# Kernel tuning notes

Measured on AMD Instinct MI355X. Metric: run time of the kernel, lower is better.

The kernel has to match this reference:

```python
import jax, jax.numpy as jnp
import numpy as np

L1, L2, L3, COUNT, B = 3072, 15, 32, 8, 16384

def setup_inputs() -> dict:
    key = jax.random.key(0)
    ks = jax.random.split(key, 10)
    s = 1.0 / np.sqrt(L1)
    inp = {
        'x': jax.random.normal(ks[0], (B, L1), dtype=jnp.float32),
        'ls_indices': jax.random.randint(ks[1], (B,), 0, COUNT, dtype=jnp.int64 if jax.config.jax_enable_x64 else jnp.int32),
        # l1: Linear(L1, (L2+1)*count)
        'l1_w': jax.random.uniform(ks[2], ((L2 + 1) * COUNT, L1), jnp.float32, -s, s),
        'l1_b': jax.random.uniform(ks[3], ((L2 + 1) * COUNT,), jnp.float32, -s, s),
        # l1_fact: Linear(L1, L2+1) -- zero-initialized in the original module
        'l1f_w': jnp.zeros((L2 + 1, L1), jnp.float32),
        'l1f_b': jnp.zeros((L2 + 1,), jnp.float32),
        # l2: Linear(2*L2, L3*count)
        'l2_w': jax.random.uniform(ks[4], (L3 * COUNT, 2 * L2), jnp.float32, -0.18, 0.18),
        'l2_b': jax.random.uniform(ks[5], (L3 * COUNT,), jnp.float32, -0.18, 0.18),
        # output: Linear(L3, count) -- bias zero-initialized
        'out_w': jax.random.uniform(ks[6], (COUNT, L3), jnp.float32, -0.176, 0.176),
        'out_b': jnp.zeros((COUNT,), jnp.float32),
    }
    return inp

def reference(x, ls_indices, l1_w, l1_b, l1f_w, l1f_b, l2_w, l2_b, out_w, out_b):
    Bn = x.shape[0]
    rows = jnp.arange(Bn)
    idx = ls_indices.astype(jnp.int32)

    # l1: compute all stacks, gather selected
    l1s = (x @ l1_w.T + l1_b).reshape(Bn, COUNT, L2 + 1)   # [B, count, 16]
    l1c = l1s[rows, idx]                                    # [B, 16]
    l1f = x @ l1f_w.T + l1f_b                               # [B, 16]
    l1c_main, l1c_out = l1c[:, :L2], l1c[:, L2:]            # [B,15],[B,1]
    l1f_main, l1f_out = l1f[:, :L2], l1f[:, L2:]

    l1x = l1c_main + l1f_main                               # [B, 15]
    l1x = jnp.clip(jnp.concatenate([jnp.square(l1x) * (127.0 / 128.0), l1x], axis=1), 0.0, 1.0)  # [B, 30]

    # l2
    l2s = (l1x @ l2_w.T + l2_b).reshape(Bn, COUNT, L3)      # [B, count, 32]
    l2x = jnp.clip(l2s[rows, idx], 0.0, 1.0)                # [B, 32]

    # output
    l3s = l2x @ out_w.T + out_b                             # [B, count]
    l3c = l3s[rows, idx][:, None]                           # [B, 1]
    return l3c + l1f_out + l1c_out                          # [B, 1]
```

## Files before the change

### kernel.cpp

```cpp
#include <hip/hip_runtime.h>
#include <hip/hip_bf16.h>

#define BATCH 16384
#define K1DIM 3072
#define NCOUNT 8
#define NO 16
#define CHUNK 256
#define NCHUNK (K1DIM / CHUNK)
#define SPB 32

typedef float f32x4 __attribute__((ext_vector_type(4)));
typedef unsigned int u32;

__host__ __device__ constexpr int brev6(int i) {
    int r = 0;
    for (int b = 0; b < 6; ++b) r |= ((i >> b) & 1) << (5 - b);
    return r;
}

__global__ __launch_bounds__(256) void k_combine(const float* __restrict__ l1w,
                                                 const float* __restrict__ l1fw,
                                                 float* __restrict__ wc) {
    int i = blockIdx.x * 256 + threadIdx.x;
    int row = i / 768;
    int col = (i - row * 768) * 4;
    int o = row & 15;
    f32x4 a = *(const f32x4*)(l1w + (size_t)row * K1DIM + col);
    f32x4 f = *(const f32x4*)(l1fw + (size_t)o * K1DIM + col);
    *(f32x4*)(wc + (size_t)row * K1DIM + col) = a + f;
}

__global__ __launch_bounds__(256) void k_bucket(const int* __restrict__ ls,
                                                int* __restrict__ counts,
                                                int* __restrict__ bucketArr) {
    __shared__ int h[NCOUNT];
    __shared__ int hbase[NCOUNT];
    int t = threadIdx.x;
    if (t < NCOUNT) h[t] = 0;
    __syncthreads();
    int i = blockIdx.x * 256 + t;
    int idx = ls[i];
    int lpos = atomicAdd(&h[idx], 1);
    __syncthreads();
    if (t < NCOUNT) hbase[t] = atomicAdd(&counts[t], h[t]);
    __syncthreads();
    bucketArr[idx * BATCH + hbase[idx] + lpos] = i;
}

__device__ __forceinline__ void stage4(const float* gbase, float* lds_linear,
                                       int wid, int lane) {
#pragma unroll
    for (int i = 0; i < 4; ++i) {
        int row = wid * 4 + i;
        const float* g = gbase + (size_t)row * K1DIM + lane * 4;
        float* l = lds_linear + row * CHUNK;
        __builtin_amdgcn_global_load_lds(
            (const __attribute__((address_space(1))) u32*)g,
            (__attribute__((address_space(3))) u32*)l, 16, 0, 0);
    }
}

__global__ __launch_bounds__(256, 2) void k_gemm(
    const float* __restrict__ x, const float* __restrict__ wc_all,
    const float* __restrict__ l1b, const float* __restrict__ l1fb,
    const int* __restrict__ bucketArr, const int* __restrict__ counts,
    float* __restrict__ y) {
    __shared__ float buf[2][NO * CHUNK];

    int cnt[NCOUNT], off[NCOUNT];
    int nblk = 0;
#pragma unroll
    for (int i = 0; i < NCOUNT; ++i) {
        cnt[i] = counts[i];
        off[i] = nblk;
        nblk += (cnt[i] + SPB - 1) / SPB;
    }
    int b = blockIdx.x;
    if (b >= nblk) return;
    int bucket = 0;
#pragma unroll
    for (int i = 1; i < NCOUNT; ++i) if (b >= off[i]) bucket = i;
    int chunkblk = b - off[bucket];
    int count = cnt[bucket];

    int t = threadIdx.x;
    int lane = t & 63;
    int wid = t >> 6;

    const int* bk = bucketArr + bucket * BATCH;
    int base = chunkblk * SPB + wid * 8;
    const float* xr[8];
#pragma unroll
    for (int j = 0; j < 8; ++j) {
        int g = min(base + j, count - 1);
        xr[j] = x + (size_t)bk[g] * K1DIM + lane * 4;
    }
    const float* wstack = wc_all + (size_t)bucket * NO * K1DIM;

    float acc0[64], acc1[64];
#pragma unroll
    for (int i = 0; i < 64; ++i) { acc0[i] = 0.f; acc1[i] = 0.f; }

    stage4(wstack, &buf[0][0], wid, lane);

    for (int it = 0; it < NCHUNK; ++it) {
        int cur = it & 1;
        __syncthreads();
        if (it + 1 < NCHUNK)
            stage4(wstack + (it + 1) * CHUNK, &buf[cur ^ 1][0], wid, lane);
        int k = it * CHUNK;
        f32x4 xv[8];
#pragma unroll
        for (int j = 0; j < 8; ++j) xv[j] = *(const f32x4*)(xr[j] + k);
        const float* lb = &buf[cur][lane * 4];
#pragma unroll
        for (int o = 0; o < NO; ++o) {
            f32x4 wv = *(const f32x4*)(lb + o * CHUNK);
#define ACCUM(A, S, J)                                                   \
            {                                                            \
                float& a_ = A[brev6((S)*16 + o)];                        \
                a_ = fmaf(xv[J].x, wv.x, a_);                            \
                a_ = fmaf(xv[J].y, wv.y, a_);                            \
                a_ = fmaf(xv[J].z, wv.z, a_);                            \
                a_ = fmaf(xv[J].w, wv.w, a_);                            \
            }
            ACCUM(acc0, 0, 0) ACCUM(acc0, 1, 1) ACCUM(acc0, 2, 2) ACCUM(acc0, 3, 3)
            ACCUM(acc1, 0, 4) ACCUM(acc1, 1, 5) ACCUM(acc1, 2, 6) ACCUM(acc1, 3, 7)
#undef ACCUM
        }
    }

#pragma unroll
    for (int st = 0; st < 6; ++st) {
        const int m = 1 << st;
        const int half = 32 >> st;
        const bool hi = (lane & m) != 0;
#pragma unroll
        for (int i = 0; i < half; ++i) {
            float mine = hi ? acc0[i] : acc0[i + half];
            float other = __shfl_xor(mine, m, 64);
            float keep = hi ? acc0[i + half] : acc0[i];
            acc0[i] = keep + other;
            float mine1 = hi ? acc1[i] : acc1[i + half];
            float other1 = __shfl_xor(mine1, m, 64);
            float keep1 = hi ? acc1[i + half] : acc1[i];
            acc1[i] = keep1 + other1;
        }
    }

    int p_s = lane >> 4;
    int p_o = lane & 15;
    float bias = l1b[bucket * NO + p_o] + l1fb[p_o];
    {
        int gp = min(base + p_s, count - 1);
        y[(size_t)bk[gp] * NO + p_o] = acc0[0] + bias;
    }
    {
        int gp = min(base + 4 + p_s, count - 1);
        y[(size_t)bk[gp] * NO + p_o] = acc1[0] + bias;
    }
}

__global__ __launch_bounds__(256) void k_tail(
    const float* __restrict__ y, const int* __restrict__ ls,
    const float* __restrict__ l2w, const float* __restrict__ l2b,
    const float* __restrict__ outw, const float* __restrict__ outb,
    float* __restrict__ out) {
    int gt = blockIdx.x * 256 + threadIdx.x;
    int s = gt >> 5;
    int o2 = gt & 31;
    int idx = ls[s];
    const f32x4* yp = (const f32x4*)(y + (size_t)s * NO);
    f32x4 a0 = yp[0], a1 = yp[1], a2 = yp[2], a3 = yp[3];
    float v[16] = {a0.x, a0.y, a0.z, a0.w, a1.x, a1.y, a1.z, a1.w,
                   a2.x, a2.y, a2.z, a2.w, a3.x, a3.y, a3.z, a3.w};
    float l1x[30];
#pragma unroll
    for (int j = 0; j < 15; ++j) {
        float tv = v[j];
        float sq = tv * tv * (127.f / 128.f);
        l1x[j] = fminf(fmaxf(sq, 0.f), 1.f);
        l1x[j + 15] = fminf(fmaxf(tv, 0.f), 1.f);
    }
    const float* wr = l2w + (size_t)idx * 32 * 30 + o2 * 30;
    float tacc = l2b[idx * 32 + o2];
#pragma unroll
    for (int j = 0; j < 15; ++j) {
        float2 wpv = *(const float2*)(wr + j * 2);
        tacc = fmaf(l1x[j * 2], wpv.x, tacc);
        tacc = fmaf(l1x[j * 2 + 1], wpv.y, tacc);
    }
    tacc = fminf(fmaxf(tacc, 0.f), 1.f);
    float r = tacc * outw[idx * 32 + o2];
#pragma unroll
    for (int m = 1; m < 32; m <<= 1) r += __shfl_xor(r, m, 64);
    if (o2 == 0) out[s] = r + outb[idx] + v[15];
}

extern "C" void kernel_launch(void* const* d_in, const int* in_sizes, int n_in,
                              void* d_out, int out_size, void* d_ws, size_t ws_size,
                              hipStream_t stream) {
    const float* x    = (const float*)d_in[0];
    const int*   ls   = (const int*)  d_in[1];
    const float* l1w  = (const float*)d_in[2];
    const float* l1b  = (const float*)d_in[3];
    const float* l1fw = (const float*)d_in[4];
    const float* l1fb = (const float*)d_in[5];
    const float* l2w  = (const float*)d_in[6];
    const float* l2b  = (const float*)d_in[7];
    const float* outw = (const float*)d_in[8];
    const float* outb = (const float*)d_in[9];
    float* out = (float*)d_out;

    char* ws = (char*)d_ws;
    float* wc       = (float*)ws;
    float* y        = (float*)(ws + 1572864);
    int*   bucketArr= (int*)(ws + 1572864 + 1048576);
    int*   counts   = (int*)(ws + 1572864 + 1048576 + 524288);

    (void)hipMemsetAsync(counts, 0, 32, stream);
    k_combine<<<384, 256, 0, stream>>>(l1w, l1fw, wc);
    k_bucket<<<BATCH / 256, 256, 0, stream>>>(ls, counts, bucketArr);
    k_gemm<<<519, 256, 0, stream>>>(x, wc, l1b, l1fb, bucketArr, counts, y);
    k_tail<<<BATCH * 32 / 256, 256, 0, stream>>>(y, ls, l2w, l2b, outw, outb, out);
}
```

Baseline: 329.0 us.

## Halve samples per block, double occupancy, and prefetch x rows one chunk ahead

Each wave now handles 4 samples instead of 8, so the accumulator array is halved. Launch bounds rise to 4 blocks per SM and the grid roughly doubles. The x loads for the next K chunk are issued before the FMAs of the current chunk, which is meant to hide global load latency. The cost is that every LDS weight chunk is reused by half as many samples, so weight traffic from LDS and L2 per sample doubles.

```diff
diff --git a/kernel.cpp b/kernel.cpp
--- a/kernel.cpp
+++ b/kernel.cpp
@@ -7,7 +7,7 @@
 #define NO 16
 #define CHUNK 256
 #define NCHUNK (K1DIM / CHUNK)
-#define SPB 32
+#define SPB 16
 
 typedef float f32x4 __attribute__((ext_vector_type(4)));
 typedef unsigned int u32;
@@ -60,7 +60,7 @@
     }
 }
 
-__global__ __launch_bounds__(256, 2) void k_gemm(
+__global__ __launch_bounds__(256, 4) void k_gemm(
     const float* __restrict__ x, const float* __restrict__ wc_all,
     const float* __restrict__ l1b, const float* __restrict__ l1fb,
     const int* __restrict__ bucketArr, const int* __restrict__ counts,
@@ -88,45 +88,53 @@
     int wid = t >> 6;
 
     const int* bk = bucketArr + bucket * BATCH;
-    int base = chunkblk * SPB + wid * 8;
-    const float* xr[8];
-#pragma unroll
-    for (int j = 0; j < 8; ++j) {
+    int base = chunkblk * SPB + wid * 4;
+    const float* xr[4];
+#pragma unroll
+    for (int j = 0; j < 4; ++j) {
         int g = min(base + j, count - 1);
         xr[j] = x + (size_t)bk[g] * K1DIM + lane * 4;
     }
     const float* wstack = wc_all + (size_t)bucket * NO * K1DIM;
 
-    float acc0[64], acc1[64];
-#pragma unroll
-    for (int i = 0; i < 64; ++i) { acc0[i] = 0.f; acc1[i] = 0.f; }
+    float acc[64];
+#pragma unroll
+    for (int i = 0; i < 64; ++i) acc[i] = 0.f;
 
     stage4(wstack, &buf[0][0], wid, lane);
+
+    f32x4 xv[4];
+#pragma unroll
+    for (int j = 0; j < 4; ++j) xv[j] = *(const f32x4*)(xr[j]);
 
     for (int it = 0; it < NCHUNK; ++it) {
         int cur = it & 1;
         __syncthreads();
-        if (it + 1 < NCHUNK)
+        f32x4 xvn[4];
+        if (it + 1 < NCHUNK) {
             stage4(wstack + (it + 1) * CHUNK, &buf[cur ^ 1][0], wid, lane);
-        int k = it * CHUNK;
-        f32x4 xv[8];
-#pragma unroll
-        for (int j = 0; j < 8; ++j) xv[j] = *(const f32x4*)(xr[j] + k);
+            int kn = (it + 1) * CHUNK;
+#pragma unroll
+            for (int j = 0; j < 4; ++j) xvn[j] = *(const f32x4*)(xr[j] + kn);
+        }
         const float* lb = &buf[cur][lane * 4];
 #pragma unroll
         for (int o = 0; o < NO; ++o) {
             f32x4 wv = *(const f32x4*)(lb + o * CHUNK);
-#define ACCUM(A, S, J)                                                   \
+#define ACCUM(S)                                                         \
             {                                                            \
-                float& a_ = A[brev6((S)*16 + o)];                        \
-                a_ = fmaf(xv[J].x, wv.x, a_);                            \
-                a_ = fmaf(xv[J].y, wv.y, a_);                            \
-                a_ = fmaf(xv[J].z, wv.z, a_);                            \
-                a_ = fmaf(xv[J].w, wv.w, a_);                            \
+                float& a_ = acc[brev6((S)*16 + o)];                      \
+                a_ = fmaf(xv[S].x, wv.x, a_);                            \
+                a_ = fmaf(xv[S].y, wv.y, a_);                            \
+                a_ = fmaf(xv[S].z, wv.z, a_);                            \
+                a_ = fmaf(xv[S].w, wv.w, a_);                            \
             }
-            ACCUM(acc0, 0, 0) ACCUM(acc0, 1, 1) ACCUM(acc0, 2, 2) ACCUM(acc0, 3, 3)
-            ACCUM(acc1, 0, 4) ACCUM(acc1, 1, 5) ACCUM(acc1, 2, 6) ACCUM(acc1, 3, 7)
+            ACCUM(0) ACCUM(1) ACCUM(2) ACCUM(3)
 #undef ACCUM
+        }
+        if (it + 1 < NCHUNK) {
+#pragma unroll
+            for (int j = 0; j < 4; ++j) xv[j] = xvn[j];
         }
     }
 
@@ -137,28 +145,19 @@
         const bool hi = (lane & m) != 0;
 #pragma unroll
         for (int i = 0; i < half; ++i) {
-            float mine = hi ? acc0[i] : acc0[i + half];
+            float mine = hi ? acc[i] : acc[i + half];
             float other = __shfl_xor(mine, m, 64);
-            float keep = hi ? acc0[i + half] : acc0[i];
-            acc0[i] = keep + other;
-            float mine1 = hi ? acc1[i] : acc1[i + half];
-            float other1 = __shfl_xor(mine1, m, 64);
-            float keep1 = hi ? acc1[i + half] : acc1[i];
-            acc1[i] = keep1 + other1;
+            float keep = hi ? acc[i + half] : acc[i];
+            acc[i] = keep + other;
         }
     }
 
     int p_s = lane >> 4;
     int p_o = lane & 15;
+    int gp = min(base + p_s, count - 1);
+    int sid = bk[gp];
     float bias = l1b[bucket * NO + p_o] + l1fb[p_o];
-    {
-        int gp = min(base + p_s, count - 1);
-        y[(size_t)bk[gp] * NO + p_o] = acc0[0] + bias;
-    }
-    {
-        int gp = min(base + 4 + p_s, count - 1);
-        y[(size_t)bk[gp] * NO + p_o] = acc1[0] + bias;
-    }
+    y[(size_t)sid * NO + p_o] = acc[0] + bias;
 }
 
 __global__ __launch_bounds__(256) void k_tail(
@@ -221,6 +220,6 @@
     (void)hipMemsetAsync(counts, 0, 32, stream);
     k_combine<<<384, 256, 0, stream>>>(l1w, l1fw, wc);
     k_bucket<<<BATCH / 256, 256, 0, stream>>>(ls, counts, bucketArr);
-    k_gemm<<<519, 256, 0, stream>>>(x, wc, l1b, l1fb, bucketArr, counts, y);
+    k_gemm<<<1031, 256, 0, stream>>>(x, wc, l1b, l1fb, bucketArr, counts, y);
     k_tail<<<BATCH * 32 / 256, 256, 0, stream>>>(y, ls, l2w, l2b, outw, outb, out);
 }
```

After: 334.3 us. Within noise of the previous version (+1.6%).
